# Kernel tuning notes

Hardware: AMD Instinct MI355X
Metric: run time of the kernel (lower is better)

The kernel has to match this reference:

```python
import jax, jax.numpy as jnp
import numpy as np

ROPE_BASE = 10000.0


def rotate_half(x):
    # interleaved rotate: (x0,x1,x2,x3,...) -> (-x1,x0,-x3,x2,...)
    x1 = x[..., ::2]
    x2 = x[..., 1::2]
    return jnp.stack((-x2, x1), axis=-1).reshape(x.shape)


def rope_cos_sin(seq_len, dim, dtype):
    inv_freq = 1.0 / (ROPE_BASE ** (jnp.arange(0, dim, 2, dtype=jnp.float32) / dim))
    pos = jnp.arange(seq_len, dtype=jnp.float32)
    freqs = jnp.outer(pos, inv_freq)              # [S, dim/2]
    emb = jnp.concatenate([freqs, freqs], axis=-1)  # [S, dim]
    return jnp.cos(emb).astype(dtype), jnp.sin(emb).astype(dtype)


def setup_inputs() -> dict:
    key = jax.random.key(0)
    k1, k2, k3, k4 = jax.random.split(key, 4)
    B, S, D = 4, 4096, 256
    scale = 1.0 / np.sqrt(D)
    x = jax.random.normal(k1, (B, S, D), dtype=jnp.float32)
    wq = jax.random.normal(k2, (D, D), dtype=jnp.float32) * scale
    wk = jax.random.normal(k3, (D, D), dtype=jnp.float32) * scale
    wv = jax.random.normal(k4, (D, D), dtype=jnp.float32) * scale
    return {"x": x, "wq": wq, "wk": wk, "wv": wv}


def reference(x, wq, wk, wv):
    D = x.shape[-1]
    S = x.shape[-2]
    # torch Linear: y = x @ W^T
    q = jnp.einsum('bsd,ed->bse', x, wq)
    k = jnp.einsum('bsd,ed->bse', x, wk)
    v = jnp.einsum('bsd,ed->bse', x, wv)
    cos, sin = rope_cos_sin(S, D, x.dtype)  # [S, D]
    q = q * cos + rotate_half(q) * sin
    k = k * cos + rotate_half(k) * sin
    scores = jnp.einsum('bqd,bkd->bqk', q, k) / jnp.sqrt(jnp.asarray(D, x.dtype))
    weights = jax.nn.softmax(scores, axis=-1)
    output = jnp.einsum('bqk,bkd->bqd', weights, v)
    return output, weights
```

## Files before the change

kernel.cpp:

```cpp
#include <hip/hip_runtime.h>
#include <hip/hip_bf16.h>
#include <stdint.h>


#define B_ 4
#define S_ 4096
#define D_ 256
#define NQ 4194304
#define NW 65536
#define NTAB 524288

typedef __attribute__((ext_vector_type(4))) float f32x4;
typedef __attribute__((ext_vector_type(8))) short short8;
typedef __attribute__((ext_vector_type(4))) short short4v;
typedef __attribute__((ext_vector_type(4))) unsigned uint32x4;

__device__ __forceinline__ short f2bf(float f) {
  unsigned u = __builtin_bit_cast(unsigned, f);
  u += 0x7fffu + ((u >> 16) & 1u);
  return (short)(u >> 16);
}
__device__ __forceinline__ float bf2f(short h) {
  unsigned u = ((unsigned)(unsigned short)h) << 16;
  return __builtin_bit_cast(float, u);
}

__device__ __forceinline__ void gload16(const void* g, void* l) {
  __builtin_amdgcn_global_load_lds(
      (const __attribute__((address_space(1))) unsigned*)g,
      (__attribute__((address_space(3))) unsigned*)l, 16, 0, 0);
}

__global__ __launch_bounds__(256) void k0_split(
    const float* __restrict__ x, const float* __restrict__ wq,
    const float* __restrict__ wk, const float* __restrict__ wv,
    short* __restrict__ xh, short* __restrict__ xl,
    short* __restrict__ wh, short* __restrict__ wl,
    float* __restrict__ ctab) {
  int idx = blockIdx.x * 256 + threadIdx.x;
  if (idx < NQ) {
    float v = x[idx];
    short hi = f2bf(v);
    xh[idx] = hi;
    xl[idx] = f2bf(v - bf2f(hi));
  } else if (idx < NQ + 3 * NW) {
    int r = idx - NQ;
    int m = r >> 16;
    int e = r & (NW - 1);
    const float* w = (m == 0) ? wq : (m == 1) ? wk : wv;
    float v = w[e];
    short hi = f2bf(v);
    wh[r] = hi;
    wl[r] = f2bf(v - bf2f(hi));
  } else {
    int t = idx - NQ - 3 * NW;
    int s = t >> 7, j = t & 127;
    float invf = __expf(-0.07195578415606394f * (float)j);
    float sn, cs;
    sincosf((float)s * invf, &sn, &cs);
    ctab[2 * t] = cs;
    ctab[2 * t + 1] = sn;
  }
}

__global__ __launch_bounds__(256) void k1_proj(
    const short* __restrict__ xh, const short* __restrict__ xl,
    const short* __restrict__ wh, const short* __restrict__ wl,
    const float* __restrict__ ctab,
    short* __restrict__ qh, short* __restrict__ ql,
    short* __restrict__ kh, short* __restrict__ kl,
    short* __restrict__ vt) {
  const int m = blockIdx.y;
  const int b = blockIdx.x >> 6;
  const int sbase = (blockIdx.x & 63) << 6;
  const int tid = threadIdx.x;
  const int w = tid >> 6;
  const int lane = tid & 63;
  const int lr = lane & 15;
  const int g = lane >> 4;

  const int srow = sbase + w * 16 + lr;
  const short* xhp = xh + ((size_t)(b * S_ + srow)) * D_;
  const short* xlp = xl + ((size_t)(b * S_ + srow)) * D_;
  const short* whm = wh + m * NW;
  const short* wlm = wl + m * NW;

  f32x4 acc[16];
#pragma unroll
  for (int i = 0; i < 16; ++i) acc[i] = (f32x4)0.f;

#pragma unroll
  for (int dc = 0; dc < 8; ++dc) {
    const int d = dc * 32 + g * 8;
    short8 ah = *(const short8*)(xhp + d);
    short8 al = *(const short8*)(xlp + d);
#pragma unroll
    for (int ct = 0; ct < 16; ++ct) {
      const int e = ct * 16 + lr;
      short8 bh = *(const short8*)(whm + e * D_ + d);
      short8 bl = *(const short8*)(wlm + e * D_ + d);
      acc[ct] = __builtin_amdgcn_mfma_f32_16x16x32_bf16(ah, bh, acc[ct], 0, 0, 0);
      acc[ct] = __builtin_amdgcn_mfma_f32_16x16x32_bf16(ah, bl, acc[ct], 0, 0, 0);
      acc[ct] = __builtin_amdgcn_mfma_f32_16x16x32_bf16(al, bh, acc[ct], 0, 0, 0);
    }
  }

  const int s0 = sbase + w * 16 + g * 4;
  if (m == 2) {
#pragma unroll
    for (int ct = 0; ct < 16; ++ct) {
      const int e = ct * 16 + lr;
      short4v pk;
#pragma unroll
      for (int r = 0; r < 4; ++r) pk[r] = f2bf(acc[ct][r]);
      *(short4v*)(vt + ((size_t)(b * D_ + e)) * S_ + s0) = pk;
    }
  } else {
    short* oh = (m == 0) ? qh : kh;
    short* ol = (m == 0) ? ql : kl;
#pragma unroll
    for (int ct = 0; ct < 16; ++ct) {
      const int e = ct * 16 + lr;
      const float sgn = (e & 1) ? 1.0f : -1.0f;
#pragma unroll
      for (int r = 0; r < 4; ++r) {
        float v = acc[ct][r];
        float p = __shfl_xor(v, 1, 64);
        const float2 cs2 = *(const float2*)(ctab + ((size_t)((s0 + r) << 7) + (e & 127)) * 2);
        float q2 = v * cs2.x + sgn * p * cs2.y;
        short hi = f2bf(q2);
        size_t off = ((size_t)(b * S_ + s0 + r)) * D_ + e;
        oh[off] = hi;
        ol[off] = f2bf(q2 - bf2f(hi));
      }
    }
  }
}

__global__ __launch_bounds__(512, 2) void k2_fused(
    const short* __restrict__ qh, const short* __restrict__ ql,
    const short* __restrict__ kh, const short* __restrict__ kl,
    const short* __restrict__ vt,
    float* __restrict__ wts, float* __restrict__ out) {
  __shared__ __align__(16) char kbuf[131072];
  __shared__ __align__(16) char etile[2][8192];
  __shared__ float part[2][64];
  __shared__ float lsum_l[64];

  const int bid = blockIdx.x;
  const int swz = (bid & 7) * 32 + (bid >> 3);
  const int b = swz >> 6;
  const int qbase = (swz & 63) << 6;
  const int tid = threadIdx.x;
  const int w = tid >> 6;
  const int lane = tid & 63;
  const int lr = lane & 15;
  const int g = lane >> 4;
  const int qg = w & 3;
  const int kg = w >> 2;
  const int qh_pv = w & 1;
  const int dh_pv = w >> 1;

  short8 qfh[8], qfl[8];
  {
    const int qrow = qbase + qg * 16 + lr;
    const short* ph = qh + ((size_t)(b * S_ + qrow)) * D_;
    const short* pl = ql + ((size_t)(b * S_ + qrow)) * D_;
#pragma unroll
    for (int dc = 0; dc < 8; ++dc) {
      qfh[dc] = *(const short8*)(ph + dc * 32 + g * 8);
      qfl[dc] = *(const short8*)(pl + dc * 32 + g * 8);
    }
  }

  f32x4 acc[2];
  acc[0] = (f32x4)0.f; acc[1] = (f32x4)0.f;
  f32x4 accv[2][4];
#pragma unroll
  for (int qt = 0; qt < 2; ++qt)
#pragma unroll
    for (int dt = 0; dt < 4; ++dt) accv[qt][dt] = (f32x4)0.f;
  float rs = 0.f;

  const char* khb = (const char*)(kh + (size_t)b * S_ * D_);
  const char* klb = (const char*)(kl + (size_t)b * S_ * D_);
  const short* vtb = vt + (size_t)b * D_ * S_;
  const int swx = (lane & 7) << 4;

  char* WB = (char*)(wts + ((size_t)(b * S_ + qbase)) * S_);
  char* EB = WB + 524288;

#pragma unroll
  for (int i = 0; i < 4; ++i) {
    const int p = i * 8192 + tid * 16;
    const int xo = p ^ (((p >> 9) & 7) << 4);
    gload16(khb + xo, kbuf + p);
    gload16(klb + xo, kbuf + 32768 + p);
  }
  __syncthreads();

  for (int kt = 0; kt < 64; ++kt) {
    const int cur = kt & 1;
    const char* kb = kbuf + cur * 65536;

    if (kt < 63) {
      const char* sh = khb + (size_t)(kt + 1) * 32768;
      const char* sl = klb + (size_t)(kt + 1) * 32768;
      char* kn = kbuf + (cur ^ 1) * 65536;
#pragma unroll
      for (int i = 0; i < 4; ++i) {
        const int p = i * 8192 + tid * 16;
        const int xo = p ^ (((p >> 9) & 7) << 4);
        gload16(sh + xo, kn + p);
        gload16(sl + xo, kn + 32768 + p);
      }
    }

    if (kt > 0) {
      const char* et = etile[cur ^ 1];
      {
        const int p = tid * 16;
        const int row = p >> 7, cb = p & 127;
        uint32x4 v = *(const uint32x4*)(et + (p ^ ((row & 7) << 4)));
        *(uint32x4*)(EB + (size_t)row * 8192 + (kt - 1) * 128 + cb) = v;
      }
      __builtin_amdgcn_s_setprio(1);
#pragma unroll
      for (int kk = 0; kk < 2; ++kk) {
        short8 ea0, ea1;
        {
          const int row = qh_pv * 32 + lr;
          ea0 = *(const short8*)(et + ((row * 128 + kk * 64 + g * 16) ^ ((row & 7) << 4)));
        }
        {
          const int row = qh_pv * 32 + 16 + lr;
          ea1 = *(const short8*)(et + ((row * 128 + kk * 64 + g * 16) ^ ((row & 7) << 4)));
        }
#pragma unroll
        for (int dt = 0; dt < 4; ++dt) {
          const int d = dh_pv * 64 + dt * 16 + lr;
          short8 vb = *(const short8*)(vtb + (size_t)d * S_ + (kt - 1) * 64 + kk * 32 + g * 8);
          accv[0][dt] = __builtin_amdgcn_mfma_f32_16x16x32_bf16(ea0, vb, accv[0][dt], 0, 0, 0);
          accv[1][dt] = __builtin_amdgcn_mfma_f32_16x16x32_bf16(ea1, vb, accv[1][dt], 0, 0, 0);
        }
      }
      __builtin_amdgcn_s_setprio(0);
    }

    __builtin_amdgcn_s_setprio(1);
#pragma unroll
    for (int dc = 0; dc < 8; ++dc) {
      short8 afh[2], afl[2];
#pragma unroll
      for (int ks = 0; ks < 2; ++ks) {
        const int row = kg * 32 + ks * 16 + lr;
        const int x = (row * 512 + dc * 64 + g * 16) ^ swx;
        afh[ks] = *(const short8*)(kb + x);
        afl[ks] = *(const short8*)(kb + 32768 + x);
      }
#pragma unroll
      for (int ks = 0; ks < 2; ++ks) {
        acc[ks] = __builtin_amdgcn_mfma_f32_16x16x32_bf16(afh[ks], qfh[dc], acc[ks], 0, 0, 0);
        acc[ks] = __builtin_amdgcn_mfma_f32_16x16x32_bf16(afh[ks], qfl[dc], acc[ks], 0, 0, 0);
        acc[ks] = __builtin_amdgcn_mfma_f32_16x16x32_bf16(afl[ks], qfh[dc], acc[ks], 0, 0, 0);
      }
    }
    __builtin_amdgcn_s_setprio(0);

#pragma unroll
    for (int ks = 0; ks < 2; ++ks) {
      f32x4 e;
#pragma unroll
      for (int r = 0; r < 4; ++r) e[r] = __expf(acc[ks][r] * 0.0625f);
      rs += e[0] + e[1] + e[2] + e[3];
      unsigned lo = (unsigned)(unsigned short)f2bf(e[0]) |
                    ((unsigned)(unsigned short)f2bf(e[1]) << 16);
      unsigned hi2 = (unsigned)(unsigned short)f2bf(e[2]) |
                     ((unsigned)(unsigned short)f2bf(e[3]) << 16);
      const int row = qg * 16 + lr;
      const int colb = (kg * 32 + ks * 16 + g * 4) * 2;
      const int ad = (row * 128 + colb) ^ ((row & 7) << 4);
      *(uint2*)(etile[cur] + ad) = make_uint2(lo, hi2);
      acc[ks] = (f32x4)0.f;
    }
    __syncthreads();
  }

  {
    const char* et = etile[1];
    {
      const int p = tid * 16;
      const int row = p >> 7, cb = p & 127;
      uint32x4 v = *(const uint32x4*)(et + (p ^ ((row & 7) << 4)));
      *(uint32x4*)(EB + (size_t)row * 8192 + 63 * 128 + cb) = v;
    }
#pragma unroll
    for (int kk = 0; kk < 2; ++kk) {
      short8 ea0, ea1;
      {
        const int row = qh_pv * 32 + lr;
        ea0 = *(const short8*)(et + ((row * 128 + kk * 64 + g * 16) ^ ((row & 7) << 4)));
      }
      {
        const int row = qh_pv * 32 + 16 + lr;
        ea1 = *(const short8*)(et + ((row * 128 + kk * 64 + g * 16) ^ ((row & 7) << 4)));
      }
#pragma unroll
      for (int dt = 0; dt < 4; ++dt) {
        const int d = dh_pv * 64 + dt * 16 + lr;
        short8 vb = *(const short8*)(vtb + (size_t)d * S_ + 63 * 64 + kk * 32 + g * 8);
        accv[0][dt] = __builtin_amdgcn_mfma_f32_16x16x32_bf16(ea0, vb, accv[0][dt], 0, 0, 0);
        accv[1][dt] = __builtin_amdgcn_mfma_f32_16x16x32_bf16(ea1, vb, accv[1][dt], 0, 0, 0);
      }
    }
  }

  rs += __shfl_xor(rs, 16, 64);
  rs += __shfl_xor(rs, 32, 64);
  if (lane < 16) part[kg][qg * 16 + lane] = rs;
  __syncthreads();
  if (tid < 64) lsum_l[tid] = part[0][tid] + part[1][tid];
  __syncthreads();

#pragma unroll
  for (int i = 0; i < 2; ++i) {
    const int p = i * 8192 + tid * 16;
    *(uint32x4*)(kbuf + p) = *(const uint32x4*)(EB + (size_t)62 * 8192 + p);
  }

  {
    float* ob = out + (size_t)b * S_ * D_;
    float rv[2][4];
#pragma unroll
    for (int qt = 0; qt < 2; ++qt)
#pragma unroll
      for (int r = 0; r < 4; ++r)
        rv[qt][r] = 1.0f / lsum_l[qh_pv * 32 + qt * 16 + g * 4 + r];
#pragma unroll
    for (int qt = 0; qt < 2; ++qt)
#pragma unroll
      for (int dt = 0; dt < 4; ++dt)
#pragma unroll
        for (int r = 0; r < 4; ++r) {
          const int q = qbase + qh_pv * 32 + qt * 16 + g * 4 + r;
          ob[(size_t)q * D_ + dh_pv * 64 + dt * 16 + lr] = accv[qt][dt][r] * rv[qt][r];
        }
  }
  __syncthreads();

  const int pr0[6] = {0, 32, 48, 56, 60, 62};
  const int pr1[6] = {32, 48, 56, 60, 62, 64};
  float* WBf = (float*)WB;
#pragma unroll 1
  for (int ph = 0; ph < 6; ++ph) {
    for (int r = pr0[ph] + w; r < pr1[ph]; r += 8) {
      const float rinv = 1.0f / lsum_l[r];
      const short* erow = (r >= 62) ? (const short*)(kbuf + (size_t)(r - 62) * 8192)
                                    : (const short*)(EB + (size_t)r * 8192);
      float* wrow = WBf + (size_t)r * 4096;
      for (int c = lane * 8; c < 4096; c += 512) {
        short8 ev = *(const short8*)(erow + c);
        f32x4 o0, o1;
#pragma unroll
        for (int j = 0; j < 4; ++j) o0[j] = bf2f(ev[j]) * rinv;
#pragma unroll
        for (int j = 0; j < 4; ++j) o1[j] = bf2f(ev[4 + j]) * rinv;
        *(f32x4*)(wrow + c) = o0;
        *(f32x4*)(wrow + c + 4) = o1;
      }
    }
    __syncthreads();
  }
}

extern "C" void kernel_launch(void* const* d_in, const int* in_sizes, int n_in,
                              void* d_out, int out_size, void* d_ws, size_t ws_size,
                              hipStream_t stream) {
  const float* x  = (const float*)d_in[0];
  const float* wq = (const float*)d_in[1];
  const float* wk = (const float*)d_in[2];
  const float* wv = (const float*)d_in[3];

  float* out = (float*)d_out;
  float* wts = out + (size_t)B_ * S_ * D_;

  short* xh = (short*)d_ws;
  short* xl = xh + NQ;
  short* qh = xl + NQ;
  short* ql = qh + NQ;
  short* kh = ql + NQ;
  short* kl = kh + NQ;
  short* vt = kl + NQ;
  short* wh = vt + NQ;
  short* wl = wh + 3 * NW;
  float* ctab = (float*)(wl + 3 * NW);

  k0_split<<<dim3((NQ + 3 * NW + NTAB) / 256), 256, 0, stream>>>(
      x, wq, wk, wv, xh, xl, wh, wl, ctab);
  k1_proj<<<dim3(B_ * S_ / 64, 3), 256, 0, stream>>>(
      xh, xl, wh, wl, ctab, qh, ql, kh, kl, vt);
  k2_fused<<<dim3(B_ * S_ / 64), 512, 0, stream>>>(
      qh, ql, kh, kl, vt, wts, out);
}
```

Before: 480.4 us.

## Halve attention query tile to 32 rows and read K-low directly from global

The fused attention kernel now handles 32 query rows per block instead of 64, which doubles the grid to 512 blocks. It also splits keys across 4 wave groups and stages only the high half of K in shared memory, with the low-precision half read straight from global memory. The goal is to cut LDS use per block (roughly 136KB down to about 72KB) so more blocks fit per CU and the larger grid fills the device better. The cost is that K/V tiles are re-read twice as often across blocks, and the K-low loads become uncoalesced global reads in the inner loop.

```diff
diff --git a/kernel.cpp b/kernel.cpp
--- a/kernel.cpp
+++ b/kernel.cpp
@@ -142,24 +142,22 @@
     const short* __restrict__ kh, const short* __restrict__ kl,
     const short* __restrict__ vt,
     float* __restrict__ wts, float* __restrict__ out) {
-  __shared__ __align__(16) char kbuf[131072];
-  __shared__ __align__(16) char etile[2][8192];
-  __shared__ float part[2][64];
-  __shared__ float lsum_l[64];
+  __shared__ __align__(16) char kbuf[65536];
+  __shared__ __align__(16) char etile[2][4096];
+  __shared__ float part[4][32];
+  __shared__ float lsum_l[32];
 
   const int bid = blockIdx.x;
-  const int swz = (bid & 7) * 32 + (bid >> 3);
-  const int b = swz >> 6;
-  const int qbase = (swz & 63) << 6;
+  const int swz = (bid & 7) * 64 + ((bid >> 3) & 31) * 2 + (bid >> 8);
+  const int b = swz >> 7;
+  const int qbase = (swz & 127) << 5;
   const int tid = threadIdx.x;
   const int w = tid >> 6;
   const int lane = tid & 63;
   const int lr = lane & 15;
   const int g = lane >> 4;
-  const int qg = w & 3;
-  const int kg = w >> 2;
-  const int qh_pv = w & 1;
-  const int dh_pv = w >> 1;
+  const int qg = w & 1;
+  const int kg = w >> 1;
 
   short8 qfh[8], qfl[8];
   {
@@ -173,13 +171,12 @@
     }
   }
 
-  f32x4 acc[2];
-  acc[0] = (f32x4)0.f; acc[1] = (f32x4)0.f;
-  f32x4 accv[2][4];
-#pragma unroll
-  for (int qt = 0; qt < 2; ++qt)
-#pragma unroll
-    for (int dt = 0; dt < 4; ++dt) accv[qt][dt] = (f32x4)0.f;
+  f32x4 acc = (f32x4)0.f;
+  f32x4 accv[2][2];
+#pragma unroll
+  for (int qs = 0; qs < 2; ++qs)
+#pragma unroll
+    for (int dt = 0; dt < 2; ++dt) accv[qs][dt] = (f32x4)0.f;
   float rs = 0.f;
 
   const char* khb = (const char*)(kh + (size_t)b * S_ * D_);
@@ -188,57 +185,54 @@
   const int swx = (lane & 7) << 4;
 
   char* WB = (char*)(wts + ((size_t)(b * S_ + qbase)) * S_);
-  char* EB = WB + 524288;
+  char* EB = WB + 262144;
 
 #pragma unroll
   for (int i = 0; i < 4; ++i) {
     const int p = i * 8192 + tid * 16;
     const int xo = p ^ (((p >> 9) & 7) << 4);
     gload16(khb + xo, kbuf + p);
-    gload16(klb + xo, kbuf + 32768 + p);
   }
   __syncthreads();
 
   for (int kt = 0; kt < 64; ++kt) {
     const int cur = kt & 1;
-    const char* kb = kbuf + cur * 65536;
+    const char* kb = kbuf + cur * 32768;
 
     if (kt < 63) {
       const char* sh = khb + (size_t)(kt + 1) * 32768;
-      const char* sl = klb + (size_t)(kt + 1) * 32768;
-      char* kn = kbuf + (cur ^ 1) * 65536;
+      char* kn = kbuf + (cur ^ 1) * 32768;
 #pragma unroll
       for (int i = 0; i < 4; ++i) {
         const int p = i * 8192 + tid * 16;
         const int xo = p ^ (((p >> 9) & 7) << 4);
         gload16(sh + xo, kn + p);
-        gload16(sl + xo, kn + 32768 + p);
       }
     }
 
     if (kt > 0) {
       const char* et = etile[cur ^ 1];
       {
-        const int p = tid * 16;
+        const int p = tid * 8;
         const int row = p >> 7, cb = p & 127;
-        uint32x4 v = *(const uint32x4*)(et + (p ^ ((row & 7) << 4)));
-        *(uint32x4*)(EB + (size_t)row * 8192 + (kt - 1) * 128 + cb) = v;
+        uint2 v = *(const uint2*)(et + (p ^ ((row & 7) << 4)));
+        *(uint2*)(EB + (size_t)row * 8192 + (kt - 1) * 128 + cb) = v;
       }
       __builtin_amdgcn_s_setprio(1);
 #pragma unroll
       for (int kk = 0; kk < 2; ++kk) {
         short8 ea0, ea1;
         {
-          const int row = qh_pv * 32 + lr;
+          const int row = lr;
           ea0 = *(const short8*)(et + ((row * 128 + kk * 64 + g * 16) ^ ((row & 7) << 4)));
         }
         {
-          const int row = qh_pv * 32 + 16 + lr;
+          const int row = 16 + lr;
           ea1 = *(const short8*)(et + ((row * 128 + kk * 64 + g * 16) ^ ((row & 7) << 4)));
         }
 #pragma unroll
-        for (int dt = 0; dt < 4; ++dt) {
-          const int d = dh_pv * 64 + dt * 16 + lr;
+        for (int dt = 0; dt < 2; ++dt) {
+          const int d = w * 32 + dt * 16 + lr;
           short8 vb = *(const short8*)(vtb + (size_t)d * S_ + (kt - 1) * 64 + kk * 32 + g * 8);
           accv[0][dt] = __builtin_amdgcn_mfma_f32_16x16x32_bf16(ea0, vb, accv[0][dt], 0, 0, 0);
           accv[1][dt] = __builtin_amdgcn_mfma_f32_16x16x32_bf16(ea1, vb, accv[1][dt], 0, 0, 0);
@@ -250,38 +244,30 @@
     __builtin_amdgcn_s_setprio(1);
 #pragma unroll
     for (int dc = 0; dc < 8; ++dc) {
-      short8 afh[2], afl[2];
-#pragma unroll
-      for (int ks = 0; ks < 2; ++ks) {
-        const int row = kg * 32 + ks * 16 + lr;
-        const int x = (row * 512 + dc * 64 + g * 16) ^ swx;
-        afh[ks] = *(const short8*)(kb + x);
-        afl[ks] = *(const short8*)(kb + 32768 + x);
-      }
-#pragma unroll
-      for (int ks = 0; ks < 2; ++ks) {
-        acc[ks] = __builtin_amdgcn_mfma_f32_16x16x32_bf16(afh[ks], qfh[dc], acc[ks], 0, 0, 0);
-        acc[ks] = __builtin_amdgcn_mfma_f32_16x16x32_bf16(afh[ks], qfl[dc], acc[ks], 0, 0, 0);
-        acc[ks] = __builtin_amdgcn_mfma_f32_16x16x32_bf16(afl[ks], qfh[dc], acc[ks], 0, 0, 0);
-      }
+      const int row = kg * 16 + lr;
+      const int x = (row * 512 + dc * 64 + g * 16) ^ swx;
+      short8 afh = *(const short8*)(kb + x);
+      short8 afl = *(const short8*)(klb + (size_t)(kt * 64 + row) * 512 + dc * 64 + g * 16);
+      acc = __builtin_amdgcn_mfma_f32_16x16x32_bf16(afh, qfh[dc], acc, 0, 0, 0);
+      acc = __builtin_amdgcn_mfma_f32_16x16x32_bf16(afh, qfl[dc], acc, 0, 0, 0);
+      acc = __builtin_amdgcn_mfma_f32_16x16x32_bf16(afl, qfh[dc], acc, 0, 0, 0);
     }
     __builtin_amdgcn_s_setprio(0);
 
-#pragma unroll
-    for (int ks = 0; ks < 2; ++ks) {
+    {
       f32x4 e;
 #pragma unroll
-      for (int r = 0; r < 4; ++r) e[r] = __expf(acc[ks][r] * 0.0625f);
+      for (int r = 0; r < 4; ++r) e[r] = __expf(acc[r] * 0.0625f);
       rs += e[0] + e[1] + e[2] + e[3];
       unsigned lo = (unsigned)(unsigned short)f2bf(e[0]) |
                     ((unsigned)(unsigned short)f2bf(e[1]) << 16);
       unsigned hi2 = (unsigned)(unsigned short)f2bf(e[2]) |
                      ((unsigned)(unsigned short)f2bf(e[3]) << 16);
       const int row = qg * 16 + lr;
-      const int colb = (kg * 32 + ks * 16 + g * 4) * 2;
+      const int colb = (kg * 16 + g * 4) * 2;
       const int ad = (row * 128 + colb) ^ ((row & 7) << 4);
       *(uint2*)(etile[cur] + ad) = make_uint2(lo, hi2);
-      acc[ks] = (f32x4)0.f;
+      acc = (f32x4)0.f;
     }
     __syncthreads();
   }
@@ -289,25 +275,25 @@
   {
     const char* et = etile[1];
     {
-      const int p = tid * 16;
+      const int p = tid * 8;
       const int row = p >> 7, cb = p & 127;
-      uint32x4 v = *(const uint32x4*)(et + (p ^ ((row & 7) << 4)));
-      *(uint32x4*)(EB + (size_t)row * 8192 + 63 * 128 + cb) = v;
+      uint2 v = *(const uint2*)(et + (p ^ ((row & 7) << 4)));
+      *(uint2*)(EB + (size_t)row * 8192 + 63 * 128 + cb) = v;
     }
 #pragma unroll
     for (int kk = 0; kk < 2; ++kk) {
       short8 ea0, ea1;
       {
-        const int row = qh_pv * 32 + lr;
+        const int row = lr;
         ea0 = *(const short8*)(et + ((row * 128 + kk * 64 + g * 16) ^ ((row & 7) << 4)));
       }
       {
-        const int row = qh_pv * 32 + 16 + lr;
+        const int row = 16 + lr;
         ea1 = *(const short8*)(et + ((row * 128 + kk * 64 + g * 16) ^ ((row & 7) << 4)));
       }
 #pragma unroll
-      for (int dt = 0; dt < 4; ++dt) {
-        const int d = dh_pv * 64 + dt * 16 + lr;
+      for (int dt = 0; dt < 2; ++dt) {
+        const int d = w * 32 + dt * 16 + lr;
         short8 vb = *(const short8*)(vtb + (size_t)d * S_ + 63 * 64 + kk * 32 + g * 8);
         accv[0][dt] = __builtin_amdgcn_mfma_f32_16x16x32_bf16(ea0, vb, accv[0][dt], 0, 0, 0);
         accv[1][dt] = __builtin_amdgcn_mfma_f32_16x16x32_bf16(ea1, vb, accv[1][dt], 0, 0, 0);
@@ -319,43 +305,44 @@
   rs += __shfl_xor(rs, 32, 64);
   if (lane < 16) part[kg][qg * 16 + lane] = rs;
   __syncthreads();
-  if (tid < 64) lsum_l[tid] = part[0][tid] + part[1][tid];
+  if (tid < 32)
+    lsum_l[tid] = part[0][tid] + part[1][tid] + part[2][tid] + part[3][tid];
   __syncthreads();
 
 #pragma unroll
   for (int i = 0; i < 2; ++i) {
     const int p = i * 8192 + tid * 16;
-    *(uint32x4*)(kbuf + p) = *(const uint32x4*)(EB + (size_t)62 * 8192 + p);
+    *(uint32x4*)(kbuf + p) = *(const uint32x4*)(EB + (size_t)30 * 8192 + p);
   }
 
   {
     float* ob = out + (size_t)b * S_ * D_;
     float rv[2][4];
 #pragma unroll
-    for (int qt = 0; qt < 2; ++qt)
+    for (int qs = 0; qs < 2; ++qs)
 #pragma unroll
       for (int r = 0; r < 4; ++r)
-        rv[qt][r] = 1.0f / lsum_l[qh_pv * 32 + qt * 16 + g * 4 + r];
-#pragma unroll
-    for (int qt = 0; qt < 2; ++qt)
-#pragma unroll
-      for (int dt = 0; dt < 4; ++dt)
+        rv[qs][r] = 1.0f / lsum_l[qs * 16 + g * 4 + r];
+#pragma unroll
+    for (int qs = 0; qs < 2; ++qs)
+#pragma unroll
+      for (int dt = 0; dt < 2; ++dt)
 #pragma unroll
         for (int r = 0; r < 4; ++r) {
-          const int q = qbase + qh_pv * 32 + qt * 16 + g * 4 + r;
-          ob[(size_t)q * D_ + dh_pv * 64 + dt * 16 + lr] = accv[qt][dt][r] * rv[qt][r];
+          const int q = qbase + qs * 16 + g * 4 + r;
+          ob[(size_t)q * D_ + w * 32 + dt * 16 + lr] = accv[qs][dt][r] * rv[qs][r];
         }
   }
   __syncthreads();
 
-  const int pr0[6] = {0, 32, 48, 56, 60, 62};
-  const int pr1[6] = {32, 48, 56, 60, 62, 64};
+  const int pr0[5] = {0, 16, 24, 28, 30};
+  const int pr1[5] = {16, 24, 28, 30, 32};
   float* WBf = (float*)WB;
 #pragma unroll 1
-  for (int ph = 0; ph < 6; ++ph) {
+  for (int ph = 0; ph < 5; ++ph) {
     for (int r = pr0[ph] + w; r < pr1[ph]; r += 8) {
       const float rinv = 1.0f / lsum_l[r];
-      const short* erow = (r >= 62) ? (const short*)(kbuf + (size_t)(r - 62) * 8192)
+      const short* erow = (r >= 30) ? (const short*)(kbuf + (size_t)(r - 30) * 8192)
                                     : (const short*)(EB + (size_t)r * 8192);
       float* wrow = WBf + (size_t)r * 4096;
       for (int c = lane * 8; c < 4096; c += 512) {
@@ -399,6 +386,6 @@
       x, wq, wk, wv, xh, xl, wh, wl, ctab);
   k1_proj<<<dim3(B_ * S_ / 64, 3), 256, 0, stream>>>(
       xh, xl, wh, wl, ctab, qh, ql, kh, kl, vt);
-  k2_fused<<<dim3(B_ * S_ / 64), 512, 0, stream>>>(
+  k2_fused<<<dim3(512), 512, 0, stream>>>(
       qh, ql, kh, kl, vt, wts, out);
 }
```

Measured after the change: 656.1 us. 1.37x slower.
